# Kernel tuning notes

Hardware: AMD Instinct MI355X
Metric: run time of the kernel (lower is better)

## Reference

```python
import jax, jax.numpy as jnp
import numpy as np

IN, H = 40, 64

def setup_inputs() -> dict:
    key = jax.random.key(0)
    ks = jax.random.split(key, 10)
    s_ih = 1.0 / np.sqrt(H)
    return {
        "x": jax.random.normal(ks[0], (1024, 500, IN), dtype=jnp.float32),
        "W_ih": jax.random.uniform(ks[1], (4 * H, IN), minval=-s_ih, maxval=s_ih, dtype=jnp.float32),
        "W_hh": jax.random.uniform(ks[2], (4 * H, H), minval=-s_ih, maxval=s_ih, dtype=jnp.float32),
        "b_ih": jax.random.uniform(ks[3], (4 * H,), minval=-s_ih, maxval=s_ih, dtype=jnp.float32),
        "b_hh": jax.random.uniform(ks[4], (4 * H,), minval=-s_ih, maxval=s_ih, dtype=jnp.float32),
        "fc1_w": jax.random.uniform(ks[5], (H, H), minval=-s_ih, maxval=s_ih, dtype=jnp.float32),
        "fc1_b": jax.random.uniform(ks[6], (H,), minval=-s_ih, maxval=s_ih, dtype=jnp.float32),
        "fc2_w": jax.random.uniform(ks[7], (2, H), minval=-s_ih, maxval=s_ih, dtype=jnp.float32),
        "fc2_b": jax.random.uniform(ks[8], (2,), minval=-s_ih, maxval=s_ih, dtype=jnp.float32),
    }

def _lstm_last_hidden(x, W_ih, W_hh, b_ih, b_hh):
    B = x.shape[0]
    # Precompute input projections for all timesteps in one big GEMM: [B,T,4H]
    x_proj = jnp.einsum('bti,gi->btg', x, W_ih) + (b_ih + b_hh)
    x_proj_t = jnp.swapaxes(x_proj, 0, 1)  # [T,B,4H] for scan over time

    def step(carry, xp):
        h, c = carry
        z = xp + h @ W_hh.T  # [B,4H], PyTorch gate order: i,f,g,o
        i = jax.nn.sigmoid(z[:, 0 * H:1 * H])
        f = jax.nn.sigmoid(z[:, 1 * H:2 * H])
        g = jnp.tanh(z[:, 2 * H:3 * H])
        o = jax.nn.sigmoid(z[:, 3 * H:4 * H])
        c = f * c + i * g
        h = o * jnp.tanh(c)
        return (h, c), None

    h0 = jnp.zeros((B, H), dtype=x.dtype)
    (h_last, _), _ = jax.lax.scan(step, (h0, h0), x_proj_t)
    return h_last  # [B,H]

def reference(x, W_ih, W_hh, b_ih, b_hh, fc1_w, fc1_b, fc2_w, fc2_b):
    h = _lstm_last_hidden(x, W_ih, W_hh, b_ih, b_hh)
    h = jax.nn.relu(h @ fc1_w.T + fc1_b)
    return h @ fc2_w.T + fc2_b  # [B,2]
```

## Files before the change

kernel.cpp:

```cpp
#include <hip/hip_runtime.h>

#define IN_DIM 40
#define HID 64
#define TSTEPS 500
#define CHAINS 16

typedef _Float16 half8 __attribute__((ext_vector_type(8)));
typedef float    f32x4 __attribute__((ext_vector_type(4)));

__device__ __forceinline__ float sigmoid_fast(float x) {
    return __builtin_amdgcn_rcpf(1.0f + __expf(-x));
}

__device__ __forceinline__ float tanh_fast(float x) {
    float ax = fabsf(x);
    float e = __expf(-2.0f * ax);
    float r = (1.0f - e) * __builtin_amdgcn_rcpf(1.0f + e);
    return copysignf(r, x);
}

__device__ __forceinline__ void block_sync_lds() {
    asm volatile("s_waitcnt lgkmcnt(0)" ::: "memory");
    __builtin_amdgcn_s_barrier();
    asm volatile("" ::: "memory");
}

__global__ __launch_bounds__(256, 1)
void lstm_mfma(const float* __restrict__ x,
               const float* __restrict__ W_ih,
               const float* __restrict__ W_hh,
               const float* __restrict__ b_ih,
               const float* __restrict__ b_hh,
               const float* __restrict__ fc1_w,
               const float* __restrict__ fc1_b,
               const float* __restrict__ fc2_w,
               const float* __restrict__ fc2_b,
               float* __restrict__ out)
{
    const int tid = threadIdx.x;
    const int w   = tid >> 6;
    const int l   = tid & 63;
    const int lr  = l & 15;
    const int lg  = l >> 4;
    const int blk = blockIdx.x;
    const int sw  = (lr & 7) << 4;

    __shared__ __align__(16) unsigned short slab[2][CHAINS][HID];
    __shared__ float h32[CHAINS][HID];
    __shared__ float rl [CHAINS][HID];

    if (tid < 128) reinterpret_cast<uint4*>(slab)[tid] = uint4{0, 0, 0, 0};

    half8 wfrag[4][4];
    f32x4 biasr[4];
    #pragma unroll
    for (int j = 0; j < 4; ++j) {
        const int jt   = 4 * w + j;
        const int unit = 4 * jt + (lr >> 2);
        const int gate = lr & 3;
        const int row  = gate * HID + unit;
        #pragma unroll
        for (int kt = 0; kt < 4; ++kt) {
            const int k0 = kt * 32 + lg * 8;
            float v[8];
            if (k0 < 64) {
                const float4* p = reinterpret_cast<const float4*>(W_hh + (size_t)row * HID + k0);
                float4 q0 = p[0], q1 = p[1];
                v[0]=q0.x; v[1]=q0.y; v[2]=q0.z; v[3]=q0.w;
                v[4]=q1.x; v[5]=q1.y; v[6]=q1.z; v[7]=q1.w;
            } else if (k0 < 104) {
                const float4* p = reinterpret_cast<const float4*>(W_ih + (size_t)row * IN_DIM + (k0 - 64));
                float4 q0 = p[0], q1 = p[1];
                v[0]=q0.x; v[1]=q0.y; v[2]=q0.z; v[3]=q0.w;
                v[4]=q1.x; v[5]=q1.y; v[6]=q1.z; v[7]=q1.w;
            } else {
                #pragma unroll
                for (int e = 0; e < 8; ++e) v[e] = 0.0f;
            }
            half8 hv;
            #pragma unroll
            for (int e = 0; e < 8; ++e) hv[e] = (_Float16)v[e];
            wfrag[j][kt] = hv;
        }
        const int ud = 4 * jt + lg;
        biasr[j] = f32x4{ b_ih[0 * HID + ud] + b_hh[0 * HID + ud],
                          b_ih[1 * HID + ud] + b_hh[1 * HID + ud],
                          b_ih[2 * HID + ud] + b_hh[2 * HID + ud],
                          b_ih[3 * HID + ud] + b_hh[3 * HID + ud] };
    }

    const float* xrow = x + ((size_t)(blk * CHAINS + lr) * TSTEPS) * IN_DIM;
    const float* xg2  = xrow + lg * 8;
    const float* xg3  = xrow + 32;

    f32x4 xaccA[4], xaccB[4];
    {
        float4 p0 = *reinterpret_cast<const float4*>(xg2);
        float4 p1 = *reinterpret_cast<const float4*>(xg2 + 4);
        float4 p2 = *reinterpret_cast<const float4*>(xg3);
        float4 p3 = *reinterpret_cast<const float4*>(xg3 + 4);
        half8 xf2 = { (_Float16)p0.x, (_Float16)p0.y, (_Float16)p0.z, (_Float16)p0.w,
                      (_Float16)p1.x, (_Float16)p1.y, (_Float16)p1.z, (_Float16)p1.w };
        half8 xf3 = { (_Float16)p2.x, (_Float16)p2.y, (_Float16)p2.z, (_Float16)p2.w,
                      (_Float16)p3.x, (_Float16)p3.y, (_Float16)p3.z, (_Float16)p3.w };
        #pragma unroll
        for (int j = 0; j < 4; ++j) {
            f32x4 a = biasr[j];
            a = __builtin_amdgcn_mfma_f32_16x16x32_f16(wfrag[j][2], xf2, a, 0, 0, 0);
            a = __builtin_amdgcn_mfma_f32_16x16x32_f16(wfrag[j][3], xf3, a, 0, 0, 0);
            xaccA[j] = a;
        }
    }
    float4 rA0 = *reinterpret_cast<const float4*>(xg2 + IN_DIM);
    float4 rA1 = *reinterpret_cast<const float4*>(xg2 + IN_DIM + 4);
    float4 rA2 = *reinterpret_cast<const float4*>(xg3 + IN_DIM);
    float4 rA3 = *reinterpret_cast<const float4*>(xg3 + IN_DIM + 4);
    float4 rB0, rB1, rB2, rB3;

    __syncthreads();

    float cs[4] = {0.f, 0.f, 0.f, 0.f};
    float hreg[4];

    auto step = [&](int t, int par, f32x4 (&xacc)[4], f32x4 (&xnxt)[4],
                    const float4& c0, const float4& c1, const float4& c2, const float4& c3,
                    float4& n0, float4& n1, float4& n2, float4& n3) {
        const bool lastt = (t == TSTEPS - 1);
        const char* sb = reinterpret_cast<const char*>(slab) + par * 2048 + lr * 128;
        uint4 q0 = *reinterpret_cast<const uint4*>(sb + ((lg * 16) ^ sw));
        uint4 q1 = *reinterpret_cast<const uint4*>(sb + ((64 + lg * 16) ^ sw));
        {
            const size_t toff = (size_t)((t + 2 < TSTEPS) ? t + 2 : TSTEPS - 1) * IN_DIM;
            n0 = *reinterpret_cast<const float4*>(xg2 + toff);
            n1 = *reinterpret_cast<const float4*>(xg2 + toff + 4);
            n2 = *reinterpret_cast<const float4*>(xg3 + toff);
            n3 = *reinterpret_cast<const float4*>(xg3 + toff + 4);
        }
        half8 bf0 = __builtin_bit_cast(half8, q0);
        half8 bf1 = __builtin_bit_cast(half8, q1);
        f32x4 acc[4];
        #pragma unroll
        for (int j = 0; j < 4; ++j) {
            f32x4 a = xacc[j];
            a = __builtin_amdgcn_mfma_f32_16x16x32_f16(wfrag[j][0], bf0, a, 0, 0, 0);
            a = __builtin_amdgcn_mfma_f32_16x16x32_f16(wfrag[j][1], bf1, a, 0, 0, 0);
            acc[j] = a;
        }
        char* db = reinterpret_cast<char*>(slab) + (par ^ 1) * 2048 + lr * 128;
        #pragma unroll
        for (int j = 0; j < 4; ++j) {
            float iv = sigmoid_fast(acc[j][0]);
            float fv = sigmoid_fast(acc[j][1]);
            float gv = tanh_fast(acc[j][2]);
            float ov = sigmoid_fast(acc[j][3]);
            cs[j]   = fmaf(fv, cs[j], iv * gv);
            hreg[j] = ov * tanh_fast(cs[j]);
            const int u = 4 * (4 * w + j) + lg;
            if (lastt) {
                h32[lr][u] = hreg[j];
            } else {
                _Float16 hf = (_Float16)hreg[j];
                *reinterpret_cast<unsigned short*>(db + ((u * 2) ^ sw)) =
                    __builtin_bit_cast(unsigned short, hf);
            }
        }
        {
            half8 xf2 = { (_Float16)c0.x, (_Float16)c0.y, (_Float16)c0.z, (_Float16)c0.w,
                          (_Float16)c1.x, (_Float16)c1.y, (_Float16)c1.z, (_Float16)c1.w };
            half8 xf3 = { (_Float16)c2.x, (_Float16)c2.y, (_Float16)c2.z, (_Float16)c2.w,
                          (_Float16)c3.x, (_Float16)c3.y, (_Float16)c3.z, (_Float16)c3.w };
            #pragma unroll
            for (int j = 0; j < 4; ++j) {
                f32x4 a = biasr[j];
                a = __builtin_amdgcn_mfma_f32_16x16x32_f16(wfrag[j][2], xf2, a, 0, 0, 0);
                a = __builtin_amdgcn_mfma_f32_16x16x32_f16(wfrag[j][3], xf3, a, 0, 0, 0);
                xnxt[j] = a;
            }
        }
        block_sync_lds();
    };

    #pragma unroll 1
    for (int t = 0; t < TSTEPS; t += 2) {
        step(t,     0, xaccA, xaccB, rA0, rA1, rA2, rA3, rB0, rB1, rB2, rB3);
        step(t + 1, 1, xaccB, xaccA, rB0, rB1, rB2, rB3, rA0, rA1, rA2, rA3);
    }

    {
        float4 wrow[16];
        const float4* fwp = reinterpret_cast<const float4*>(fc1_w + (size_t)l * HID);
        #pragma unroll
        for (int q = 0; q < 16; ++q) wrow[q] = fwp[q];
        const float b1 = fc1_b[l];
        #pragma unroll
        for (int cc = 0; cc < 4; ++cc) {
            const int chain = 4 * w + cc;
            float acc = b1;
            #pragma unroll
            for (int q = 0; q < 16; ++q) {
                float4 hv = reinterpret_cast<const float4*>(&h32[chain][0])[q];
                acc = fmaf(wrow[q].x, hv.x, acc);
                acc = fmaf(wrow[q].y, hv.y, acc);
                acc = fmaf(wrow[q].z, hv.z, acc);
                acc = fmaf(wrow[q].w, hv.w, acc);
            }
            rl[chain][l] = fmaxf(acc, 0.0f);
        }
    }
    __syncthreads();
    if (tid < 32) {
        const int c = tid >> 1;
        const int o = tid & 1;
        float acc = fc2_b[o];
        for (int k = 0; k < HID; ++k)
            acc = fmaf(fc2_w[o * HID + k], rl[c][k], acc);
        out[(size_t)(blk * CHAINS + c) * 2 + o] = acc;
    }
}

extern "C" void kernel_launch(void* const* d_in, const int* in_sizes, int n_in,
                              void* d_out, int out_size, void* d_ws, size_t ws_size,
                              hipStream_t stream) {
    const float* x     = (const float*)d_in[0];
    const float* W_ih  = (const float*)d_in[1];
    const float* W_hh  = (const float*)d_in[2];
    const float* b_ih  = (const float*)d_in[3];
    const float* b_hh  = (const float*)d_in[4];
    const float* fc1_w = (const float*)d_in[5];
    const float* fc1_b = (const float*)d_in[6];
    const float* fc2_w = (const float*)d_in[7];
    const float* fc2_b = (const float*)d_in[8];
    float* out = (float*)d_out;

    const int B = in_sizes[0] / (TSTEPS * IN_DIM);
    lstm_mfma<<<B / CHAINS, 256, 0, stream>>>(x, W_ih, W_hh, b_ih, b_hh,
                                              fc1_w, fc1_b, fc2_w, fc2_b, out);
}
```

Measured before the change: 300.3 us.

## Process four sequences per block, replicated across MFMA columns, to spread work across more CUs

Each block now handles 4 batch sequences instead of 16, so 256 blocks are launched instead of 64. Each sequence is replicated four times across the 16 MFMA columns. Each lane now computes only one gate unit's nonlinearity, picked from the accumulators with selects, rather than four. The hidden state is written to four replicated LDS rows, padded to 144 bytes instead of using the XOR swizzle. The intent is to fill the GPU's CUs and shorten the serial per-step critical path, at the cost of redundant MFMA work and more LDS writes.

```diff
diff --git a/kernel.cpp b/kernel.cpp
--- a/kernel.cpp
+++ b/kernel.cpp
@@ -3,7 +3,9 @@
 #define IN_DIM 40
 #define HID 64
 #define TSTEPS 500
-#define CHAINS 16
+#define NCH 4
+#define ROWB 144
+#define SLABP (16 * ROWB)
 
 typedef _Float16 half8 __attribute__((ext_vector_type(8)));
 typedef float    f32x4 __attribute__((ext_vector_type(4)));
@@ -42,14 +44,15 @@
     const int l   = tid & 63;
     const int lr  = l & 15;
     const int lg  = l >> 4;
+    const int ch  = lr & 3;
+    const int jj  = lr >> 2;
     const int blk = blockIdx.x;
-    const int sw  = (lr & 7) << 4;
-
-    __shared__ __align__(16) unsigned short slab[2][CHAINS][HID];
-    __shared__ float h32[CHAINS][HID];
-    __shared__ float rl [CHAINS][HID];
-
-    if (tid < 128) reinterpret_cast<uint4*>(slab)[tid] = uint4{0, 0, 0, 0};
+
+    __shared__ __align__(16) unsigned char slab[2 * SLABP];
+    __shared__ float h32[NCH][HID];
+    __shared__ float rl [NCH][HID];
+
+    if (tid < SLABP / 16) reinterpret_cast<uint4*>(slab)[tid] = uint4{0, 0, 0, 0};
 
     half8 wfrag[4][4];
     f32x4 biasr[4];
@@ -89,7 +92,7 @@
                           b_ih[3 * HID + ud] + b_hh[3 * HID + ud] };
     }
 
-    const float* xrow = x + ((size_t)(blk * CHAINS + lr) * TSTEPS) * IN_DIM;
+    const float* xrow = x + ((size_t)(blk * NCH + ch) * TSTEPS) * IN_DIM;
     const float* xg2  = xrow + lg * 8;
     const float* xg3  = xrow + 32;
 
@@ -119,16 +122,16 @@
 
     __syncthreads();
 
-    float cs[4] = {0.f, 0.f, 0.f, 0.f};
-    float hreg[4];
+    float cs = 0.0f;
+    const int uown = 16 * w + 4 * jj + lg;
 
     auto step = [&](int t, int par, f32x4 (&xacc)[4], f32x4 (&xnxt)[4],
                     const float4& c0, const float4& c1, const float4& c2, const float4& c3,
                     float4& n0, float4& n1, float4& n2, float4& n3) {
         const bool lastt = (t == TSTEPS - 1);
-        const char* sb = reinterpret_cast<const char*>(slab) + par * 2048 + lr * 128;
-        uint4 q0 = *reinterpret_cast<const uint4*>(sb + ((lg * 16) ^ sw));
-        uint4 q1 = *reinterpret_cast<const uint4*>(sb + ((64 + lg * 16) ^ sw));
+        const unsigned char* sb = slab + par * SLABP + lr * ROWB;
+        uint4 q0 = *reinterpret_cast<const uint4*>(sb + lg * 16);
+        uint4 q1 = *reinterpret_cast<const uint4*>(sb + 64 + lg * 16);
         {
             const size_t toff = (size_t)((t + 2 < TSTEPS) ? t + 2 : TSTEPS - 1) * IN_DIM;
             n0 = *reinterpret_cast<const float4*>(xg2 + toff);
@@ -146,23 +149,38 @@
             a = __builtin_amdgcn_mfma_f32_16x16x32_f16(wfrag[j][1], bf1, a, 0, 0, 0);
             acc[j] = a;
         }
-        char* db = reinterpret_cast<char*>(slab) + (par ^ 1) * 2048 + lr * 128;
-        #pragma unroll
-        for (int j = 0; j < 4; ++j) {
-            float iv = sigmoid_fast(acc[j][0]);
-            float fv = sigmoid_fast(acc[j][1]);
-            float gv = tanh_fast(acc[j][2]);
-            float ov = sigmoid_fast(acc[j][3]);
-            cs[j]   = fmaf(fv, cs[j], iv * gv);
-            hreg[j] = ov * tanh_fast(cs[j]);
-            const int u = 4 * (4 * w + j) + lg;
-            if (lastt) {
-                h32[lr][u] = hreg[j];
-            } else {
-                _Float16 hf = (_Float16)hreg[j];
-                *reinterpret_cast<unsigned short*>(db + ((u * 2) ^ sw)) =
-                    __builtin_bit_cast(unsigned short, hf);
-            }
+        float z0, z1, z2, z3;
+        {
+            float t01, t23;
+            t01 = (jj & 1) ? acc[1][0] : acc[0][0];
+            t23 = (jj & 1) ? acc[3][0] : acc[2][0];
+            z0  = (jj & 2) ? t23 : t01;
+            t01 = (jj & 1) ? acc[1][1] : acc[0][1];
+            t23 = (jj & 1) ? acc[3][1] : acc[2][1];
+            z1  = (jj & 2) ? t23 : t01;
+            t01 = (jj & 1) ? acc[1][2] : acc[0][2];
+            t23 = (jj & 1) ? acc[3][2] : acc[2][2];
+            z2  = (jj & 2) ? t23 : t01;
+            t01 = (jj & 1) ? acc[1][3] : acc[0][3];
+            t23 = (jj & 1) ? acc[3][3] : acc[2][3];
+            z3  = (jj & 2) ? t23 : t01;
+        }
+        float iv = sigmoid_fast(z0);
+        float fv = sigmoid_fast(z1);
+        float gv = tanh_fast(z2);
+        float ov = sigmoid_fast(z3);
+        cs = fmaf(fv, cs, iv * gv);
+        float h = ov * tanh_fast(cs);
+        if (lastt) {
+            h32[ch][uown] = h;
+        } else {
+            unsigned char* db = slab + (par ^ 1) * SLABP + uown * 2;
+            _Float16 hf = (_Float16)h;
+            unsigned short hb = __builtin_bit_cast(unsigned short, hf);
+            *reinterpret_cast<unsigned short*>(db + (ch     ) * ROWB) = hb;
+            *reinterpret_cast<unsigned short*>(db + (ch +  4) * ROWB) = hb;
+            *reinterpret_cast<unsigned short*>(db + (ch +  8) * ROWB) = hb;
+            *reinterpret_cast<unsigned short*>(db + (ch + 12) * ROWB) = hb;
         }
         {
             half8 xf2 = { (_Float16)c0.x, (_Float16)c0.y, (_Float16)c0.z, (_Float16)c0.w,
@@ -187,34 +205,27 @@
     }
 
     {
-        float4 wrow[16];
+        float acc = fc1_b[l];
         const float4* fwp = reinterpret_cast<const float4*>(fc1_w + (size_t)l * HID);
         #pragma unroll
-        for (int q = 0; q < 16; ++q) wrow[q] = fwp[q];
-        const float b1 = fc1_b[l];
-        #pragma unroll
-        for (int cc = 0; cc < 4; ++cc) {
-            const int chain = 4 * w + cc;
-            float acc = b1;
-            #pragma unroll
-            for (int q = 0; q < 16; ++q) {
-                float4 hv = reinterpret_cast<const float4*>(&h32[chain][0])[q];
-                acc = fmaf(wrow[q].x, hv.x, acc);
-                acc = fmaf(wrow[q].y, hv.y, acc);
-                acc = fmaf(wrow[q].z, hv.z, acc);
-                acc = fmaf(wrow[q].w, hv.w, acc);
-            }
-            rl[chain][l] = fmaxf(acc, 0.0f);
-        }
+        for (int q = 0; q < 16; ++q) {
+            float4 wv = fwp[q];
+            float4 hv = reinterpret_cast<const float4*>(&h32[w][0])[q];
+            acc = fmaf(wv.x, hv.x, acc);
+            acc = fmaf(wv.y, hv.y, acc);
+            acc = fmaf(wv.z, hv.z, acc);
+            acc = fmaf(wv.w, hv.w, acc);
+        }
+        rl[w][l] = fmaxf(acc, 0.0f);
     }
     __syncthreads();
-    if (tid < 32) {
+    if (tid < NCH * 2) {
         const int c = tid >> 1;
         const int o = tid & 1;
         float acc = fc2_b[o];
         for (int k = 0; k < HID; ++k)
             acc = fmaf(fc2_w[o * HID + k], rl[c][k], acc);
-        out[(size_t)(blk * CHAINS + c) * 2 + o] = acc;
+        out[(size_t)(blk * NCH + c) * 2 + o] = acc;
     }
 }
 
@@ -233,6 +244,6 @@
     float* out = (float*)d_out;
 
     const int B = in_sizes[0] / (TSTEPS * IN_DIM);
-    lstm_mfma<<<B / CHAINS, 256, 0, stream>>>(x, W_ih, W_hh, b_ih, b_hh,
-                                              fc1_w, fc1_b, fc2_w, fc2_b, out);
-}
+    lstm_mfma<<<B / NCH, 256, 0, stream>>>(x, W_ih, W_hh, b_ih, b_hh,
+                                           fc1_w, fc1_b, fc2_w, fc2_b, out);
+}
```

New measurement: 253.7 us. 15.5% less time.
